# Kernel tuning notes

Hardware: AMD Instinct MI355X
Metric: run time of the kernel (lower is better)

Reference implementation:

```python
import jax, jax.numpy as jnp
import numpy as np

B, N, M, D, H = 4, 512, 4096, 256, 8
HD = D // H


def setup_inputs() -> dict:
    key = jax.random.key(0)
    ks = jax.random.split(key, 10)
    s = 1.0 / np.sqrt(D)
    return {
        "amr_feats": jax.random.normal(ks[0], (B, N, D), jnp.float32),
        "amr_pad_mask": jax.random.randint(ks[1], (B, N), 0, 2) == 1,
        "visual_feats": jax.random.normal(ks[2], (B, M, D), jnp.float32),
        "W_amr_qk": jax.random.normal(ks[3], (D, D), jnp.float32) * s,
        "W_amr_v": jax.random.normal(ks[4], (D, D), jnp.float32) * s,
        "W_vis_qk": jax.random.normal(ks[5], (D, D), jnp.float32) * s,
        "W_vis_v": jax.random.normal(ks[6], (D, D), jnp.float32) * s,
        "W_amr_out": jax.random.normal(ks[7], (D, D), jnp.float32) * s,
        "b_amr_out": jnp.zeros((D,), jnp.float32),
        "W_vis_out": jax.random.normal(ks[8], (D, D), jnp.float32) * s,
        "b_vis_out": jnp.zeros((D,), jnp.float32),
    }


def _split_heads(x):  # [b, s, d] -> [b, h, s, hd]
    b, s, _ = x.shape
    return x.reshape(b, s, H, HD).transpose(0, 2, 1, 3)


def _merge_heads(x):  # [b, h, s, hd] -> [b, s, d]
    b, _, s, _ = x.shape
    return x.transpose(0, 2, 1, 3).reshape(b, s, H * HD)


def reference(amr_feats, amr_pad_mask, visual_feats,
              W_amr_qk, W_amr_v, W_vis_qk, W_vis_v,
              W_amr_out, b_amr_out, W_vis_out, b_vis_out):
    scale = HD ** -0.5
    amr_qk = _split_heads(amr_feats @ W_amr_qk)      # [b,h,n,hd]
    vis_qk = _split_heads(visual_feats @ W_vis_qk)   # [b,h,m,hd]
    amr_v = _split_heads(amr_feats @ W_amr_v)        # [b,h,n,hd]
    vis_v = _split_heads(visual_feats @ W_vis_v)     # [b,h,m,hd]

    # shared score matrix, computed once and reused for both directions
    common = jnp.einsum('bhnc,bhmc->bhnm', amr_qk, vis_qk) * scale  # [b,h,n,m]

    # amr -> visual (visual_pads is None in the top-level forward: no mask)
    amr_vis_w = jax.nn.softmax(common, axis=-1)
    amr_feats_2 = _merge_heads(jnp.einsum('bhnm,bhmc->bhnc', amr_vis_w, vis_v))
    amr_feats_2 = amr_feats_2 @ W_amr_out + b_amr_out

    # visual -> amr, masked by amr_pad_mask
    neg = jnp.finfo(common.dtype).min
    vis_txt = jnp.where(amr_pad_mask[:, None, None, :], neg,
                        common.transpose(0, 1, 3, 2))  # [b,h,m,n]
    vis_txt_w = jax.nn.softmax(vis_txt, axis=-1)
    visual_feats_2 = _merge_heads(jnp.einsum('bhmn,bhnc->bhmc', vis_txt_w, amr_v))
    visual_feats_2 = visual_feats_2 @ W_vis_out + b_vis_out

    # text_trans == 'dot', visual_trans == 'dot'
    return amr_feats_2 * amr_feats, visual_feats * visual_feats_2
```

## Files before the change

### kernel.cpp

```cpp
#include <hip/hip_runtime.h>

#define BB 4
#define NN 512
#define MM 4096
#define DD 256
#define HH 8
#define HDD 32

typedef __attribute__((ext_vector_type(8))) short bf16x8;
typedef __attribute__((ext_vector_type(4))) float f32x4;
typedef __attribute__((ext_vector_type(4))) unsigned int u32x4;

__device__ __forceinline__ unsigned short f2b(float f) {
    union { float f; unsigned u; } v; v.f = f;
    unsigned r = v.u + 0x7fffu + ((v.u >> 16) & 1u);
    return (unsigned short)(r >> 16);
}
__device__ __forceinline__ float b2f(unsigned short u) {
    union { unsigned u; float f; } v; v.u = ((unsigned)u) << 16;
    return v.f;
}
__device__ __forceinline__ unsigned cvt_pk_bf16(float lo, float hi) {
    unsigned r;
    asm("v_cvt_pk_bf16_f32 %0, %1, %2" : "=v"(r) : "v"(lo), "v"(hi));
    return r;
}

struct WPack { const float* s[6]; unsigned short* d[6]; };
__global__ __launch_bounds__(256) void convert_w(WPack p)
{
    __shared__ unsigned short T[64][72];
    const int mat = blockIdx.x >> 4;
    const int tile = blockIdx.x & 15;
    const int kt = (tile >> 2) * 64, ct = (tile & 3) * 64;
    const int t = threadIdx.x;
    const int kl = t >> 2, cseg = (t & 3) * 16;

    const float* src = &p.s[mat][(size_t)(kt + kl) * DD + ct + cseg];
    #pragma unroll
    for (int j4 = 0; j4 < 4; ++j4) {
        const float4 f = *(const float4*)(src + j4 * 4);
        T[cseg + j4 * 4 + 0][kl] = f2b(f.x);
        T[cseg + j4 * 4 + 1][kl] = f2b(f.y);
        T[cseg + j4 * 4 + 2][kl] = f2b(f.z);
        T[cseg + j4 * 4 + 3][kl] = f2b(f.w);
    }
    __syncthreads();
    unsigned short* dst = &p.d[mat][(size_t)(ct + kl) * DD + kt + cseg];
    *(bf16x8*)dst       = *(const bf16x8*)&T[kl][cseg];
    *(bf16x8*)(dst + 8) = *(const bf16x8*)&T[kl][cseg + 8];
}

template<int OUTMODE>
__device__ __forceinline__ void gemm_tile_in(
    const float* __restrict__ A,
    const unsigned short* __restrict__ Wt,
    float outscale,
    unsigned short* __restrict__ Cb,
    unsigned short* __restrict__ VT, int SEQ,
    const int* __restrict__ rowmask,
    int r0, int c0,
    unsigned short (*As)[72], unsigned short (*Ws)[72])
{
    const int tid = threadIdx.x;
    const int lane = tid & 63, w = tid >> 6;
    const int rq = (w >> 1) * 32, cq = (w & 1) * 32;
    const int srow = tid >> 2, skc = (tid & 3) * 16;
    const int g = lane >> 4, cl = lane & 15;

    f32x4 acc[2][2] = {};

    for (int ks = 0; ks < DD; ks += 64) {
        __syncthreads();
        {
            const float* ga = &A[(size_t)(r0 + srow) * DD + ks + skc];
            const float4 f0 = *(const float4*)(ga);
            const float4 f1 = *(const float4*)(ga + 4);
            const float4 f2 = *(const float4*)(ga + 8);
            const float4 f3 = *(const float4*)(ga + 12);
            uint4 u0, u1;
            u0.x = cvt_pk_bf16(f0.x, f0.y); u0.y = cvt_pk_bf16(f0.z, f0.w);
            u0.z = cvt_pk_bf16(f1.x, f1.y); u0.w = cvt_pk_bf16(f1.z, f1.w);
            u1.x = cvt_pk_bf16(f2.x, f2.y); u1.y = cvt_pk_bf16(f2.z, f2.w);
            u1.z = cvt_pk_bf16(f3.x, f3.y); u1.w = cvt_pk_bf16(f3.z, f3.w);
            *(uint4*)&As[srow][skc]     = u0;
            *(uint4*)&As[srow][skc + 8] = u1;
            const unsigned short* gw = &Wt[(size_t)(c0 + srow) * DD + ks + skc];
            *(bf16x8*)&Ws[srow][skc]     = *(const bf16x8*)gw;
            *(bf16x8*)&Ws[srow][skc + 8] = *(const bf16x8*)(gw + 8);
        }
        __syncthreads();
        #pragma unroll
        for (int kh = 0; kh < 2; ++kh) {
            const int kk = kh * 32 + g * 8;
            const bf16x8 a0 = *(const bf16x8*)&As[rq + cl][kk];
            const bf16x8 a1 = *(const bf16x8*)&As[rq + 16 + cl][kk];
            const bf16x8 b0 = *(const bf16x8*)&Ws[cq + cl][kk];
            const bf16x8 b1 = *(const bf16x8*)&Ws[cq + 16 + cl][kk];
            acc[0][0] = __builtin_amdgcn_mfma_f32_16x16x32_bf16(a0, b0, acc[0][0], 0, 0, 0);
            acc[0][1] = __builtin_amdgcn_mfma_f32_16x16x32_bf16(a0, b1, acc[0][1], 0, 0, 0);
            acc[1][0] = __builtin_amdgcn_mfma_f32_16x16x32_bf16(a1, b0, acc[1][0], 0, 0, 0);
            acc[1][1] = __builtin_amdgcn_mfma_f32_16x16x32_bf16(a1, b1, acc[1][1], 0, 0, 0);
        }
    }

    if (OUTMODE == 0) {
        const int b0 = r0 / SEQ, mbase = r0 % SEQ;
        #pragma unroll
        for (int sr = 0; sr < 2; ++sr)
        #pragma unroll
        for (int sc = 0; sc < 2; ++sc) {
            const int col = c0 + cq + sc * 16 + cl;
            const int head = col >> 5, c32 = col & 31;
            #pragma unroll
            for (int reg = 0; reg < 4; ++reg) {
                const int m = mbase + rq + sr * 16 + g * 4 + reg;
                Cb[(((size_t)b0 * HH + head) * SEQ + m) * 32 + c32]
                    = f2b(acc[sr][sc][reg] * outscale);
            }
        }
    } else {
        const int b0 = r0 / SEQ, mbase = r0 % SEQ;
        if (rowmask != nullptr) {
            #pragma unroll
            for (int sr = 0; sr < 2; ++sr)
                #pragma unroll
                for (int reg = 0; reg < 4; ++reg) {
                    const int m = mbase + rq + sr * 16 + g * 4 + reg;
                    const float k = rowmask[b0 * SEQ + m] ? 0.f : 1.f;
                    acc[sr][0][reg] *= k;
                    acc[sr][1][reg] *= k;
                }
        }
        __syncthreads();
        #pragma unroll
        for (int sr = 0; sr < 2; ++sr)
        #pragma unroll
        for (int sc = 0; sc < 2; ++sc) {
            const int col_local = cq + sc * 16 + cl;
            uint2 u;
            u.x = cvt_pk_bf16(acc[sr][sc][0], acc[sr][sc][1]);
            u.y = cvt_pk_bf16(acc[sr][sc][2], acc[sr][sc][3]);
            *(uint2*)&As[col_local][rq + g * 8 + sr * 4] = u;
        }
        __syncthreads();
        const int col = tid >> 2, seg = tid & 3;
        unsigned short* dst = &VT[((size_t)b0 * DD + c0 + col) * SEQ + mbase + seg * 16];
        *(bf16x8*)dst       = *(const bf16x8*)&As[col][seg * 16];
        *(bf16x8*)(dst + 8) = *(const bf16x8*)&As[col][seg * 16 + 8];
    }
}

struct InPack {
    const float* amr; const float* vis;
    const unsigned short *Wqa, *Wva, *Wqv, *Wvv;
    unsigned short *amr_qk, *vis_qk, *VTa, *VTv;
    const int* mask;
    unsigned short* keepP;
    float sqs;
};
__global__ __launch_bounds__(256) void gemm_in(InPack p)
{
    __shared__ unsigned short As[64][72];
    __shared__ unsigned short Ws[64][72];
    const int bx = blockIdx.x;
    const int c0 = blockIdx.y * 64;
    if (bx < 32)
        gemm_tile_in<0>(p.amr, p.Wqa, p.sqs, p.amr_qk, nullptr, NN, nullptr, bx * 64, c0, As, Ws);
    else if (bx < 64)
        gemm_tile_in<2>(p.amr, p.Wva, 1.f, nullptr, p.VTa, NN, p.mask, (bx - 32) * 64, c0, As, Ws);
    else if (bx < 320)
        gemm_tile_in<0>(p.vis, p.Wqv, p.sqs, p.vis_qk, nullptr, MM, nullptr, (bx - 64) * 64, c0, As, Ws);
    else if (bx < 576)
        gemm_tile_in<2>(p.vis, p.Wvv, 1.f, nullptr, p.VTv, MM, nullptr, (bx - 320) * 64, c0, As, Ws);
    else if (blockIdx.y == 0) {
        #pragma unroll
        for (int k8 = 0; k8 < 8; ++k8) {
            const int idx = k8 * 256 + threadIdx.x;
            const int m = idx & (NN - 1);
            const int r = m & 31;
            const int pp = ((r & 15) >> 2) * 8 + (r >> 4) * 4 + (r & 3);
            p.keepP[(idx & ~(NN - 1)) | (m & ~31) | pp]
                = p.mask[idx] ? (unsigned short)0 : (unsigned short)0x3F80;
        }
    }
}

__device__ __forceinline__ void gemm_tile_out(
    const unsigned short* __restrict__ A,
    const unsigned short* __restrict__ Wt,
    const float* __restrict__ bias,
    const float* __restrict__ feats,
    float* __restrict__ Cf,
    int r0, int c0,
    unsigned short (*As)[72], unsigned short (*Ws)[72])
{
    const int tid = threadIdx.x;
    const int lane = tid & 63, w = tid >> 6;
    const int rq = (w >> 1) * 32, cq = (w & 1) * 32;
    const int srow = tid >> 2, skc = (tid & 3) * 16;
    const int g = lane >> 4, cl = lane & 15;

    f32x4 acc[2][2] = {};

    for (int ks = 0; ks < DD; ks += 64) {
        __syncthreads();
        {
            const unsigned short* ga = &A[(size_t)(r0 + srow) * DD + ks + skc];
            *(bf16x8*)&As[srow][skc]     = *(const bf16x8*)ga;
            *(bf16x8*)&As[srow][skc + 8] = *(const bf16x8*)(ga + 8);
            const unsigned short* gw = &Wt[(size_t)(c0 + srow) * DD + ks + skc];
            *(bf16x8*)&Ws[srow][skc]     = *(const bf16x8*)gw;
            *(bf16x8*)&Ws[srow][skc + 8] = *(const bf16x8*)(gw + 8);
        }
        __syncthreads();
        #pragma unroll
        for (int kh = 0; kh < 2; ++kh) {
            const int kk = kh * 32 + g * 8;
            const bf16x8 a0 = *(const bf16x8*)&As[rq + cl][kk];
            const bf16x8 a1 = *(const bf16x8*)&As[rq + 16 + cl][kk];
            const bf16x8 b0 = *(const bf16x8*)&Ws[cq + cl][kk];
            const bf16x8 b1 = *(const bf16x8*)&Ws[cq + 16 + cl][kk];
            acc[0][0] = __builtin_amdgcn_mfma_f32_16x16x32_bf16(a0, b0, acc[0][0], 0, 0, 0);
            acc[0][1] = __builtin_amdgcn_mfma_f32_16x16x32_bf16(a0, b1, acc[0][1], 0, 0, 0);
            acc[1][0] = __builtin_amdgcn_mfma_f32_16x16x32_bf16(a1, b0, acc[1][0], 0, 0, 0);
            acc[1][1] = __builtin_amdgcn_mfma_f32_16x16x32_bf16(a1, b1, acc[1][1], 0, 0, 0);
        }
    }

    #pragma unroll
    for (int sr = 0; sr < 2; ++sr)
    #pragma unroll
    for (int sc = 0; sc < 2; ++sc) {
        const int col = c0 + cq + sc * 16 + cl;
        #pragma unroll
        for (int reg = 0; reg < 4; ++reg) {
            const int row = r0 + rq + sr * 16 + g * 4 + reg;
            const size_t idx = (size_t)row * DD + col;
            Cf[idx] = (acc[sr][sc][reg] + bias[col]) * feats[idx];
        }
    }
}

struct OutPack {
    const unsigned short* A[2];
    const unsigned short* Wt[2];
    const float* bias[2];
    const float* feats[2];
    float* O[2];
};
__global__ __launch_bounds__(256) void gemm_out(OutPack p)
{
    __shared__ unsigned short As[64][72];
    __shared__ unsigned short Ws[64][72];
    const int bx = blockIdx.x;
    const int which = (bx < 32) ? 0 : 1;
    const int rb = (bx < 32) ? bx : bx - 32;
    gemm_tile_out(p.A[which], p.Wt[which], p.bias[which], p.feats[which],
                  p.O[which], rb * 64, blockIdx.y * 64, As, Ws);
}

template<int SEQK, int SPLIT, bool HAS_KEEP>
__device__ __forceinline__ void attn_body(
    int bid,
    const unsigned short* __restrict__ Qb,
    const unsigned short* __restrict__ Kb,
    const unsigned short* __restrict__ VTb,
    const unsigned short* __restrict__ keepP,
    unsigned short* __restrict__ ctx,
    float* __restrict__ Pl, unsigned short* __restrict__ PaccB,
    int NQ)
{
    constexpr int KCHUNK = SEQK / SPLIT;
    constexpr int NT = KCHUNK / 64;

    const int tid = threadIdx.x;
    const int lane = tid & 63, w = tid >> 6;
    const int g = lane >> 4, cl = lane & 15;

    const int nqt = NQ / 256;
    int bi = bid;
    const int sp = bi % SPLIT; bi /= SPLIT;
    const int qt = bi % nqt;   bi /= nqt;
    const int h  = bi % HH;
    const int b  = bi / HH;
    const int q0 = qt * 256 + w * 64;
    const int kv0 = sp * KCHUNK;

    bf16x8 aq[4];
    #pragma unroll
    for (int qg = 0; qg < 4; ++qg)
        aq[qg] = *(const bf16x8*)
            &Qb[(((size_t)b * HH + h) * NQ + q0 + qg * 16 + cl) * 32 + g * 8];

    const unsigned short* Kp0 = Kb + (((size_t)b * HH + h) * SEQK + kv0 + cl) * 32 + g * 8;
    const unsigned short* Vp0 = VTb + ((size_t)b * DD + h * HDD + cl) * SEQK + kv0 + g * 8;
    const unsigned short* Op0 = HAS_KEEP ? (keepP + (size_t)b * SEQK + kv0 + g * 8) : nullptr;

    union { u32x4 u; bf16x8 b; } onesc;
    onesc.u[0] = 0x3F803F80u; onesc.u[1] = 0x3F803F80u;
    onesc.u[2] = 0x3F803F80u; onesc.u[3] = 0x3F803F80u;

    f32x4 acc[4][2] = {};
    f32x4 acc_l[4] = {};

    bf16x8 Kc[4], Kn[4];
    #pragma unroll
    for (int kf = 0; kf < 4; ++kf)
        Kc[kf] = *(const bf16x8*)(Kp0 + (size_t)(kf * 16) * 32);

    for (int t = 0; t < NT; ++t) {
        if (t + 1 < NT) {
            const unsigned short* kp = Kp0 + (size_t)((t + 1) * 64) * 32;
            #pragma unroll
            for (int kf = 0; kf < 4; ++kf)
                Kn[kf] = *(const bf16x8*)(kp + (size_t)(kf * 16) * 32);
        }

        bf16x8 vv[2][2];
        #pragma unroll
        for (int mh = 0; mh < 2; ++mh)
            #pragma unroll
            for (int sub = 0; sub < 2; ++sub)
                vv[mh][sub] = *(const bf16x8*)
                    (Vp0 + (size_t)(sub * 16) * SEQK + t * 64 + mh * 32);

        bf16x8 ofrag[2];
        if (HAS_KEEP) {
            ofrag[0] = *(const bf16x8*)(Op0 + t * 64);
            ofrag[1] = *(const bf16x8*)(Op0 + t * 64 + 32);
        } else {
            ofrag[0] = onesc.b;
            ofrag[1] = onesc.b;
        }

        uint2 X[4][4];
        #pragma unroll
        for (int kh = 0; kh < 2; ++kh) {
            f32x4 s[4][2];
            #pragma unroll
            for (int k2 = 0; k2 < 2; ++k2) {
                const f32x4 z = {0.f, 0.f, 0.f, 0.f};
                const bf16x8 kfrag = Kc[kh * 2 + k2];
                #pragma unroll
                for (int qg = 0; qg < 4; ++qg)
                    s[qg][k2] = __builtin_amdgcn_mfma_f32_16x16x32_bf16(
                        kfrag, aq[qg], z, 0, 0, 0);
            }
            #pragma unroll
            for (int k2 = 0; k2 < 2; ++k2) {
                const int kf = kh * 2 + k2;
                #pragma unroll
                for (int qg = 0; qg < 4; ++qg) {
                    const float p0 = exp2f(s[qg][k2][0]);
                    const float p1 = exp2f(s[qg][k2][1]);
                    const float p2 = exp2f(s[qg][k2][2]);
                    const float p3 = exp2f(s[qg][k2][3]);
                    X[qg][kf].x = cvt_pk_bf16(p0, p1);
                    X[qg][kf].y = cvt_pk_bf16(p2, p3);
                }
            }
        }

        #pragma unroll
        for (int mh = 0; mh < 2; ++mh) {
            union { u32x4 u; bf16x8 b; } pa[4];
            #pragma unroll
            for (int qg = 0; qg < 4; ++qg) {
                pa[qg].u[0] = X[qg][mh * 2].x;
                pa[qg].u[1] = X[qg][mh * 2].y;
                pa[qg].u[2] = X[qg][mh * 2 + 1].x;
                pa[qg].u[3] = X[qg][mh * 2 + 1].y;
            }
            #pragma unroll
            for (int sub = 0; sub < 2; ++sub)
                #pragma unroll
                for (int qg = 0; qg < 4; ++qg)
                    acc[qg][sub] = __builtin_amdgcn_mfma_f32_16x16x32_bf16(
                        pa[qg].b, vv[mh][sub], acc[qg][sub], 0, 0, 0);
            #pragma unroll
            for (int qg = 0; qg < 4; ++qg)
                acc_l[qg] = __builtin_amdgcn_mfma_f32_16x16x32_bf16(
                    pa[qg].b, ofrag[mh], acc_l[qg], 0, 0, 0);
        }

        #pragma unroll
        for (int kf = 0; kf < 4; ++kf) Kc[kf] = Kn[kf];
    }

    if (SPLIT > 1) {
        const int pb = bid;
        #pragma unroll
        for (int qg = 0; qg < 4; ++qg) {
            #pragma unroll
            for (int sub = 0; sub < 2; ++sub)
                #pragma unroll
                for (int reg = 0; reg < 4; ++reg) {
                    const int wq = w * 64 + qg * 16 + g * 4 + reg;
                    PaccB[((size_t)pb * 256 + wq) * 32 + sub * 16 + cl]
                        = f2b(acc[qg][sub][reg]);
                }
            if (cl == 0) {
                #pragma unroll
                for (int reg = 0; reg < 4; ++reg)
                    Pl[(size_t)pb * 256 + w * 64 + qg * 16 + g * 4 + reg]
                        = acc_l[qg][reg];
            }
        }
    } else {
        #pragma unroll
        for (int qg = 0; qg < 4; ++qg)
            #pragma unroll
            for (int sub = 0; sub < 2; ++sub)
                #pragma unroll
                for (int reg = 0; reg < 4; ++reg) {
                    const int q = q0 + qg * 16 + g * 4 + reg;
                    ctx[((size_t)b * NQ + q) * DD + h * HDD + sub * 16 + cl]
                        = f2b(acc[qg][sub][reg] / acc_l[qg][reg]);
                }
    }
}

__global__ __launch_bounds__(256) void attn_fused(
    const unsigned short* __restrict__ amr_qk,
    const unsigned short* __restrict__ vis_qk,
    const unsigned short* __restrict__ VT_vis,
    const unsigned short* __restrict__ VT_amr,
    const unsigned short* __restrict__ keepP,
    unsigned short* __restrict__ ctx1,
    float* __restrict__ Pl, unsigned short* __restrict__ PaccB)
{
    if ((blockIdx.x & 1) == 0) {
        attn_body<MM, 8, false>(blockIdx.x >> 1, amr_qk, vis_qk, VT_vis, nullptr,
                                nullptr, Pl, PaccB, NN);
    } else {
        attn_body<NN, 1, true>(blockIdx.x >> 1, vis_qk, amr_qk, VT_amr, keepP,
                               ctx1, nullptr, nullptr, MM);
    }
}

__global__ __launch_bounds__(256) void combine_split(
    const float* __restrict__ Pl, const unsigned short* __restrict__ PaccB,
    unsigned short* __restrict__ ctx)
{
    const int q = threadIdx.x;
    const int bqt = blockIdx.x;
    const int qt = bqt & 1, h = (bqt >> 1) & 7, b = bqt >> 4;
    const int pb0 = bqt * 8;

    float denom = 0.f;
    float o[32] = {};
    #pragma unroll
    for (int sp = 0; sp < 8; ++sp) {
        const size_t base = ((size_t)(pb0 + sp) * 256 + q) * 32;
        #pragma unroll
        for (int c8 = 0; c8 < 4; ++c8) {
            const bf16x8 a = *(const bf16x8*)&PaccB[base + c8 * 8];
            #pragma unroll
            for (int j = 0; j < 8; ++j)
                o[c8 * 8 + j] += b2f((unsigned short)a[j]);
        }
        denom += Pl[(size_t)(pb0 + sp) * 256 + q];
    }
    const float inv = 1.f / denom;

    unsigned short* dst = &ctx[((size_t)b * NN + qt * 256 + q) * DD + h * HDD];
    #pragma unroll
    for (int j4 = 0; j4 < 8; ++j4) {
        ushort4 u;
        u.x = f2b(o[j4 * 4 + 0] * inv); u.y = f2b(o[j4 * 4 + 1] * inv);
        u.z = f2b(o[j4 * 4 + 2] * inv); u.w = f2b(o[j4 * 4 + 3] * inv);
        *(ushort4*)(dst + j4 * 4) = u;
    }
}

extern "C" void kernel_launch(void* const* d_in, const int* in_sizes, int n_in,
                              void* d_out, int out_size, void* d_ws, size_t ws_size,
                              hipStream_t stream)
{
    const float* amr_feats    = (const float*)d_in[0];
    const int*   amr_pad_mask = (const int*)d_in[1];
    const float* visual_feats = (const float*)d_in[2];
    const float* W_amr_qk     = (const float*)d_in[3];
    const float* W_amr_v      = (const float*)d_in[4];
    const float* W_vis_qk     = (const float*)d_in[5];
    const float* W_vis_v      = (const float*)d_in[6];
    const float* W_amr_out    = (const float*)d_in[7];
    const float* b_amr_out    = (const float*)d_in[8];
    const float* W_vis_out    = (const float*)d_in[9];
    const float* b_vis_out    = (const float*)d_in[10];

    unsigned short* ws = (unsigned short*)d_ws;
    unsigned short* Wt_amr_qk  = ws;
    unsigned short* Wt_amr_v   = ws + 65536;
    unsigned short* Wt_vis_qk  = ws + 131072;
    unsigned short* Wt_vis_v   = ws + 196608;
    unsigned short* Wt_amr_out = ws + 262144;
    unsigned short* Wt_vis_out = ws + 327680;
    unsigned short* amr_qk_b   = ws + 393216;
    unsigned short* VT_amr     = ws + 917504;
    unsigned short* vis_qk_b   = ws + 1441792;
    unsigned short* VT_vis     = ws + 5636096;
    unsigned short* ctx0_b     = ws + 9830400;
    unsigned short* ctx1_b     = ws + 10354688;
    float* Pl                  = (float*)(ws + 14548992);
    unsigned short* PaccB      = ws + 15073280;
    unsigned short* keepP      = ws + 19267584;

    float* out0 = (float*)d_out;
    float* out1 = out0 + (size_t)BB * NN * DD;

    const float SQS = 0.50500976f;

    WPack wp;
    wp.s[0] = W_amr_qk;  wp.d[0] = Wt_amr_qk;
    wp.s[1] = W_amr_v;   wp.d[1] = Wt_amr_v;
    wp.s[2] = W_vis_qk;  wp.d[2] = Wt_vis_qk;
    wp.s[3] = W_vis_v;   wp.d[3] = Wt_vis_v;
    wp.s[4] = W_amr_out; wp.d[4] = Wt_amr_out;
    wp.s[5] = W_vis_out; wp.d[5] = Wt_vis_out;
    convert_w<<<96, 256, 0, stream>>>(wp);

    InPack ip;
    ip.amr = amr_feats; ip.vis = visual_feats;
    ip.Wqa = Wt_amr_qk; ip.Wva = Wt_amr_v;
    ip.Wqv = Wt_vis_qk; ip.Wvv = Wt_vis_v;
    ip.amr_qk = amr_qk_b; ip.vis_qk = vis_qk_b;
    ip.VTa = VT_amr; ip.VTv = VT_vis;
    ip.mask = amr_pad_mask; ip.keepP = keepP;
    ip.sqs = SQS;
    gemm_in<<<dim3(577, 4), 256, 0, stream>>>(ip);

    attn_fused<<<1024, 256, 0, stream>>>(
        amr_qk_b, vis_qk_b, VT_vis, VT_amr, keepP, ctx1_b, Pl, PaccB);
    combine_split<<<64, 256, 0, stream>>>(Pl, PaccB, ctx0_b);

    OutPack op;
    op.A[0] = ctx0_b; op.Wt[0] = Wt_amr_out; op.bias[0] = b_amr_out;
    op.feats[0] = amr_feats;    op.O[0] = out0;
    op.A[1] = ctx1_b; op.Wt[1] = Wt_vis_out; op.bias[1] = b_vis_out;
    op.feats[1] = visual_feats; op.O[1] = out1;
    gemm_out<<<dim3(288, 4), 256, 0, stream>>>(op);
}
```

Baseline: 91.85 us.

## Fuse QK/V input projections per tile and shrink attention blocks to one wave

The input projection kernel now computes the QK and V projections in the same block, loading and converting each activation tile once and running two weight tiles against it. The attention kernel goes from 256-thread blocks covering 256 queries to 64-thread single-wave blocks covering 64 queries, with four times as many blocks, and the exp/convert is interleaved per k-half instead of buffered. The combine kernel is reshaped to match, with each thread handling an 8-column slice. This cuts redundant activation reads and raises block-level parallelism and scheduling flexibility, at the cost of more register pressure in the fused GEMM and more, smaller blocks. The visual-side attention path (attn_body with NQ=MM) may also be affected by the nqt change, which could be inconsistent with code not shown.

```diff
diff --git a/kernel.cpp b/kernel.cpp
--- a/kernel.cpp
+++ b/kernel.cpp
@@ -51,24 +51,55 @@
     *(bf16x8*)(dst + 8) = *(const bf16x8*)&T[kl][cseg + 8];
 }
 
-template<int OUTMODE>
-__device__ __forceinline__ void gemm_tile_in(
-    const float* __restrict__ A,
-    const unsigned short* __restrict__ Wt,
-    float outscale,
-    unsigned short* __restrict__ Cb,
-    unsigned short* __restrict__ VT, int SEQ,
-    const int* __restrict__ rowmask,
-    int r0, int c0,
-    unsigned short (*As)[72], unsigned short (*Ws)[72])
-{
+struct InPack {
+    const float* amr; const float* vis;
+    const unsigned short *Wqa, *Wva, *Wqv, *Wvv;
+    unsigned short *amr_qk, *vis_qk, *VTa, *VTv;
+    const int* mask;
+    unsigned short* keepP;
+    float sqs;
+};
+__global__ __launch_bounds__(256) void gemm_in(InPack p)
+{
+    __shared__ unsigned short As[64][72];
+    __shared__ unsigned short Wq[64][72];
+    __shared__ unsigned short Wv[64][72];
+
+    const int bx = blockIdx.x;
+    if (bx == 288) {
+        if (blockIdx.y == 0) {
+            #pragma unroll
+            for (int k8 = 0; k8 < 8; ++k8) {
+                const int idx = k8 * 256 + threadIdx.x;
+                const int m = idx & (NN - 1);
+                const int r = m & 31;
+                const int pp = ((r & 15) >> 2) * 8 + (r >> 4) * 4 + (r & 3);
+                p.keepP[(idx & ~(NN - 1)) | (m & ~31) | pp]
+                    = p.mask[idx] ? (unsigned short)0 : (unsigned short)0x3F80;
+            }
+        }
+        return;
+    }
+
+    const float* A; const unsigned short *Wqm, *Wvm;
+    unsigned short *Cq, *VT; const int* rowmask; int SEQ, r0;
+    if (bx < 32) {
+        A = p.amr; Wqm = p.Wqa; Wvm = p.Wva; Cq = p.amr_qk; VT = p.VTa;
+        rowmask = p.mask; SEQ = NN; r0 = bx * 64;
+    } else {
+        A = p.vis; Wqm = p.Wqv; Wvm = p.Wvv; Cq = p.vis_qk; VT = p.VTv;
+        rowmask = nullptr; SEQ = MM; r0 = (bx - 32) * 64;
+    }
+    const int c0 = blockIdx.y * 64;
+
     const int tid = threadIdx.x;
     const int lane = tid & 63, w = tid >> 6;
     const int rq = (w >> 1) * 32, cq = (w & 1) * 32;
     const int srow = tid >> 2, skc = (tid & 3) * 16;
     const int g = lane >> 4, cl = lane & 15;
 
-    f32x4 acc[2][2] = {};
+    f32x4 aq[2][2] = {};
+    f32x4 av[2][2] = {};
 
     for (int ks = 0; ks < DD; ks += 64) {
         __syncthreads();
@@ -85,6 +116,104 @@
             u1.z = cvt_pk_bf16(f3.x, f3.y); u1.w = cvt_pk_bf16(f3.z, f3.w);
             *(uint4*)&As[srow][skc]     = u0;
             *(uint4*)&As[srow][skc + 8] = u1;
+            const unsigned short* gq = &Wqm[(size_t)(c0 + srow) * DD + ks + skc];
+            *(bf16x8*)&Wq[srow][skc]     = *(const bf16x8*)gq;
+            *(bf16x8*)&Wq[srow][skc + 8] = *(const bf16x8*)(gq + 8);
+            const unsigned short* gv = &Wvm[(size_t)(c0 + srow) * DD + ks + skc];
+            *(bf16x8*)&Wv[srow][skc]     = *(const bf16x8*)gv;
+            *(bf16x8*)&Wv[srow][skc + 8] = *(const bf16x8*)(gv + 8);
+        }
+        __syncthreads();
+        #pragma unroll
+        for (int kh = 0; kh < 2; ++kh) {
+            const int kk = kh * 32 + g * 8;
+            const bf16x8 a0 = *(const bf16x8*)&As[rq + cl][kk];
+            const bf16x8 a1 = *(const bf16x8*)&As[rq + 16 + cl][kk];
+            const bf16x8 q0 = *(const bf16x8*)&Wq[cq + cl][kk];
+            const bf16x8 q1 = *(const bf16x8*)&Wq[cq + 16 + cl][kk];
+            const bf16x8 v0 = *(const bf16x8*)&Wv[cq + cl][kk];
+            const bf16x8 v1 = *(const bf16x8*)&Wv[cq + 16 + cl][kk];
+            aq[0][0] = __builtin_amdgcn_mfma_f32_16x16x32_bf16(a0, q0, aq[0][0], 0, 0, 0);
+            aq[0][1] = __builtin_amdgcn_mfma_f32_16x16x32_bf16(a0, q1, aq[0][1], 0, 0, 0);
+            aq[1][0] = __builtin_amdgcn_mfma_f32_16x16x32_bf16(a1, q0, aq[1][0], 0, 0, 0);
+            aq[1][1] = __builtin_amdgcn_mfma_f32_16x16x32_bf16(a1, q1, aq[1][1], 0, 0, 0);
+            av[0][0] = __builtin_amdgcn_mfma_f32_16x16x32_bf16(a0, v0, av[0][0], 0, 0, 0);
+            av[0][1] = __builtin_amdgcn_mfma_f32_16x16x32_bf16(a0, v1, av[0][1], 0, 0, 0);
+            av[1][0] = __builtin_amdgcn_mfma_f32_16x16x32_bf16(a1, v0, av[1][0], 0, 0, 0);
+            av[1][1] = __builtin_amdgcn_mfma_f32_16x16x32_bf16(a1, v1, av[1][1], 0, 0, 0);
+        }
+    }
+
+    const int b0 = r0 / SEQ, mbase = r0 % SEQ;
+
+    #pragma unroll
+    for (int sr = 0; sr < 2; ++sr)
+    #pragma unroll
+    for (int sc = 0; sc < 2; ++sc) {
+        const int col = c0 + cq + sc * 16 + cl;
+        const int head = col >> 5, c32 = col & 31;
+        #pragma unroll
+        for (int reg = 0; reg < 4; ++reg) {
+            const int m = mbase + rq + sr * 16 + g * 4 + reg;
+            Cq[(((size_t)b0 * HH + head) * SEQ + m) * 32 + c32]
+                = f2b(aq[sr][sc][reg] * p.sqs);
+        }
+    }
+
+    if (rowmask != nullptr) {
+        #pragma unroll
+        for (int sr = 0; sr < 2; ++sr)
+            #pragma unroll
+            for (int reg = 0; reg < 4; ++reg) {
+                const int m = mbase + rq + sr * 16 + g * 4 + reg;
+                const float k = rowmask[b0 * SEQ + m] ? 0.f : 1.f;
+                av[sr][0][reg] *= k;
+                av[sr][1][reg] *= k;
+            }
+    }
+    __syncthreads();
+    #pragma unroll
+    for (int sr = 0; sr < 2; ++sr)
+    #pragma unroll
+    for (int sc = 0; sc < 2; ++sc) {
+        const int col_local = cq + sc * 16 + cl;
+        uint2 u;
+        u.x = cvt_pk_bf16(av[sr][sc][0], av[sr][sc][1]);
+        u.y = cvt_pk_bf16(av[sr][sc][2], av[sr][sc][3]);
+        *(uint2*)&As[col_local][rq + g * 8 + sr * 4] = u;
+    }
+    __syncthreads();
+    {
+        const int col = tid >> 2, seg = tid & 3;
+        unsigned short* dst = &VT[((size_t)b0 * DD + c0 + col) * SEQ + mbase + seg * 16];
+        *(bf16x8*)dst       = *(const bf16x8*)&As[col][seg * 16];
+        *(bf16x8*)(dst + 8) = *(const bf16x8*)&As[col][seg * 16 + 8];
+    }
+}
+
+__device__ __forceinline__ void gemm_tile_out(
+    const unsigned short* __restrict__ A,
+    const unsigned short* __restrict__ Wt,
+    const float* __restrict__ bias,
+    const float* __restrict__ feats,
+    float* __restrict__ Cf,
+    int r0, int c0,
+    unsigned short (*As)[72], unsigned short (*Ws)[72])
+{
+    const int tid = threadIdx.x;
+    const int lane = tid & 63, w = tid >> 6;
+    const int rq = (w >> 1) * 32, cq = (w & 1) * 32;
+    const int srow = tid >> 2, skc = (tid & 3) * 16;
+    const int g = lane >> 4, cl = lane & 15;
+
+    f32x4 acc[2][2] = {};
+
+    for (int ks = 0; ks < DD; ks += 64) {
+        __syncthreads();
+        {
+            const unsigned short* ga = &A[(size_t)(r0 + srow) * DD + ks + skc];
+            *(bf16x8*)&As[srow][skc]     = *(const bf16x8*)ga;
+            *(bf16x8*)&As[srow][skc + 8] = *(const bf16x8*)(ga + 8);
             const unsigned short* gw = &Wt[(size_t)(c0 + srow) * DD + ks + skc];
             *(bf16x8*)&Ws[srow][skc]     = *(const bf16x8*)gw;
             *(bf16x8*)&Ws[srow][skc + 8] = *(const bf16x8*)(gw + 8);
@@ -104,130 +233,6 @@
         }
     }
 
-    if (OUTMODE == 0) {
-        const int b0 = r0 / SEQ, mbase = r0 % SEQ;
-        #pragma unroll
-        for (int sr = 0; sr < 2; ++sr)
-        #pragma unroll
-        for (int sc = 0; sc < 2; ++sc) {
-            const int col = c0 + cq + sc * 16 + cl;
-            const int head = col >> 5, c32 = col & 31;
-            #pragma unroll
-            for (int reg = 0; reg < 4; ++reg) {
-                const int m = mbase + rq + sr * 16 + g * 4 + reg;
-                Cb[(((size_t)b0 * HH + head) * SEQ + m) * 32 + c32]
-                    = f2b(acc[sr][sc][reg] * outscale);
-            }
-        }
-    } else {
-        const int b0 = r0 / SEQ, mbase = r0 % SEQ;
-        if (rowmask != nullptr) {
-            #pragma unroll
-            for (int sr = 0; sr < 2; ++sr)
-                #pragma unroll
-                for (int reg = 0; reg < 4; ++reg) {
-                    const int m = mbase + rq + sr * 16 + g * 4 + reg;
-                    const float k = rowmask[b0 * SEQ + m] ? 0.f : 1.f;
-                    acc[sr][0][reg] *= k;
-                    acc[sr][1][reg] *= k;
-                }
-        }
-        __syncthreads();
-        #pragma unroll
-        for (int sr = 0; sr < 2; ++sr)
-        #pragma unroll
-        for (int sc = 0; sc < 2; ++sc) {
-            const int col_local = cq + sc * 16 + cl;
-            uint2 u;
-            u.x = cvt_pk_bf16(acc[sr][sc][0], acc[sr][sc][1]);
-            u.y = cvt_pk_bf16(acc[sr][sc][2], acc[sr][sc][3]);
-            *(uint2*)&As[col_local][rq + g * 8 + sr * 4] = u;
-        }
-        __syncthreads();
-        const int col = tid >> 2, seg = tid & 3;
-        unsigned short* dst = &VT[((size_t)b0 * DD + c0 + col) * SEQ + mbase + seg * 16];
-        *(bf16x8*)dst       = *(const bf16x8*)&As[col][seg * 16];
-        *(bf16x8*)(dst + 8) = *(const bf16x8*)&As[col][seg * 16 + 8];
-    }
-}
-
-struct InPack {
-    const float* amr; const float* vis;
-    const unsigned short *Wqa, *Wva, *Wqv, *Wvv;
-    unsigned short *amr_qk, *vis_qk, *VTa, *VTv;
-    const int* mask;
-    unsigned short* keepP;
-    float sqs;
-};
-__global__ __launch_bounds__(256) void gemm_in(InPack p)
-{
-    __shared__ unsigned short As[64][72];
-    __shared__ unsigned short Ws[64][72];
-    const int bx = blockIdx.x;
-    const int c0 = blockIdx.y * 64;
-    if (bx < 32)
-        gemm_tile_in<0>(p.amr, p.Wqa, p.sqs, p.amr_qk, nullptr, NN, nullptr, bx * 64, c0, As, Ws);
-    else if (bx < 64)
-        gemm_tile_in<2>(p.amr, p.Wva, 1.f, nullptr, p.VTa, NN, p.mask, (bx - 32) * 64, c0, As, Ws);
-    else if (bx < 320)
-        gemm_tile_in<0>(p.vis, p.Wqv, p.sqs, p.vis_qk, nullptr, MM, nullptr, (bx - 64) * 64, c0, As, Ws);
-    else if (bx < 576)
-        gemm_tile_in<2>(p.vis, p.Wvv, 1.f, nullptr, p.VTv, MM, nullptr, (bx - 320) * 64, c0, As, Ws);
-    else if (blockIdx.y == 0) {
-        #pragma unroll
-        for (int k8 = 0; k8 < 8; ++k8) {
-            const int idx = k8 * 256 + threadIdx.x;
-            const int m = idx & (NN - 1);
-            const int r = m & 31;
-            const int pp = ((r & 15) >> 2) * 8 + (r >> 4) * 4 + (r & 3);
-            p.keepP[(idx & ~(NN - 1)) | (m & ~31) | pp]
-                = p.mask[idx] ? (unsigned short)0 : (unsigned short)0x3F80;
-        }
-    }
-}
-
-__device__ __forceinline__ void gemm_tile_out(
-    const unsigned short* __restrict__ A,
-    const unsigned short* __restrict__ Wt,
-    const float* __restrict__ bias,
-    const float* __restrict__ feats,
-    float* __restrict__ Cf,
-    int r0, int c0,
-    unsigned short (*As)[72], unsigned short (*Ws)[72])
-{
-    const int tid = threadIdx.x;
-    const int lane = tid & 63, w = tid >> 6;
-    const int rq = (w >> 1) * 32, cq = (w & 1) * 32;
-    const int srow = tid >> 2, skc = (tid & 3) * 16;
-    const int g = lane >> 4, cl = lane & 15;
-
-    f32x4 acc[2][2] = {};
-
-    for (int ks = 0; ks < DD; ks += 64) {
-        __syncthreads();
-        {
-            const unsigned short* ga = &A[(size_t)(r0 + srow) * DD + ks + skc];
-            *(bf16x8*)&As[srow][skc]     = *(const bf16x8*)ga;
-            *(bf16x8*)&As[srow][skc + 8] = *(const bf16x8*)(ga + 8);
-            const unsigned short* gw = &Wt[(size_t)(c0 + srow) * DD + ks + skc];
-            *(bf16x8*)&Ws[srow][skc]     = *(const bf16x8*)gw;
-            *(bf16x8*)&Ws[srow][skc + 8] = *(const bf16x8*)(gw + 8);
-        }
-        __syncthreads();
-        #pragma unroll
-        for (int kh = 0; kh < 2; ++kh) {
-            const int kk = kh * 32 + g * 8;
-            const bf16x8 a0 = *(const bf16x8*)&As[rq + cl][kk];
-            const bf16x8 a1 = *(const bf16x8*)&As[rq + 16 + cl][kk];
-            const bf16x8 b0 = *(const bf16x8*)&Ws[cq + cl][kk];
-            const bf16x8 b1 = *(const bf16x8*)&Ws[cq + 16 + cl][kk];
-            acc[0][0] = __builtin_amdgcn_mfma_f32_16x16x32_bf16(a0, b0, acc[0][0], 0, 0, 0);
-            acc[0][1] = __builtin_amdgcn_mfma_f32_16x16x32_bf16(a0, b1, acc[0][1], 0, 0, 0);
-            acc[1][0] = __builtin_amdgcn_mfma_f32_16x16x32_bf16(a1, b0, acc[1][0], 0, 0, 0);
-            acc[1][1] = __builtin_amdgcn_mfma_f32_16x16x32_bf16(a1, b1, acc[1][1], 0, 0, 0);
-        }
-    }
-
     #pragma unroll
     for (int sr = 0; sr < 2; ++sr)
     #pragma unroll
@@ -274,17 +279,16 @@
     constexpr int KCHUNK = SEQK / SPLIT;
     constexpr int NT = KCHUNK / 64;
 
-    const int tid = threadIdx.x;
-    const int lane = tid & 63, w = tid >> 6;
+    const int lane = threadIdx.x & 63;
     const int g = lane >> 4, cl = lane & 15;
 
-    const int nqt = NQ / 256;
+    const int nqt = NQ / 64;
     int bi = bid;
     const int sp = bi % SPLIT; bi /= SPLIT;
     const int qt = bi % nqt;   bi /= nqt;
     const int h  = bi % HH;
     const int b  = bi / HH;
-    const int q0 = qt * 256 + w * 64;
+    const int q0 = qt * 64;
     const int kv0 = sp * KCHUNK;
 
     bf16x8 aq[4];
@@ -334,7 +338,6 @@
             ofrag[1] = onesc.b;
         }
 
-        uint2 X[4][4];
         #pragma unroll
         for (int kh = 0; kh < 2; ++kh) {
             f32x4 s[4][2];
@@ -347,41 +350,24 @@
                     s[qg][k2] = __builtin_amdgcn_mfma_f32_16x16x32_bf16(
                         kfrag, aq[qg], z, 0, 0, 0);
             }
-            #pragma unroll
-            for (int k2 = 0; k2 < 2; ++k2) {
-                const int kf = kh * 2 + k2;
-                #pragma unroll
-                for (int qg = 0; qg < 4; ++qg) {
-                    const float p0 = exp2f(s[qg][k2][0]);
-                    const float p1 = exp2f(s[qg][k2][1]);
-                    const float p2 = exp2f(s[qg][k2][2]);
-                    const float p3 = exp2f(s[qg][k2][3]);
-                    X[qg][kf].x = cvt_pk_bf16(p0, p1);
-                    X[qg][kf].y = cvt_pk_bf16(p2, p3);
-                }
-            }
-        }
-
-        #pragma unroll
-        for (int mh = 0; mh < 2; ++mh) {
             union { u32x4 u; bf16x8 b; } pa[4];
             #pragma unroll
             for (int qg = 0; qg < 4; ++qg) {
-                pa[qg].u[0] = X[qg][mh * 2].x;
-                pa[qg].u[1] = X[qg][mh * 2].y;
-                pa[qg].u[2] = X[qg][mh * 2 + 1].x;
-                pa[qg].u[3] = X[qg][mh * 2 + 1].y;
+                pa[qg].u[0] = cvt_pk_bf16(exp2f(s[qg][0][0]), exp2f(s[qg][0][1]));
+                pa[qg].u[1] = cvt_pk_bf16(exp2f(s[qg][0][2]), exp2f(s[qg][0][3]));
+                pa[qg].u[2] = cvt_pk_bf16(exp2f(s[qg][1][0]), exp2f(s[qg][1][1]));
+                pa[qg].u[3] = cvt_pk_bf16(exp2f(s[qg][1][2]), exp2f(s[qg][1][3]));
             }
             #pragma unroll
             for (int sub = 0; sub < 2; ++sub)
                 #pragma unroll
                 for (int qg = 0; qg < 4; ++qg)
                     acc[qg][sub] = __builtin_amdgcn_mfma_f32_16x16x32_bf16(
-                        pa[qg].b, vv[mh][sub], acc[qg][sub], 0, 0, 0);
+                        pa[qg].b, vv[kh][sub], acc[qg][sub], 0, 0, 0);
             #pragma unroll
             for (int qg = 0; qg < 4; ++qg)
                 acc_l[qg] = __builtin_amdgcn_mfma_f32_16x16x32_bf16(
-                    pa[qg].b, ofrag[mh], acc_l[qg], 0, 0, 0);
+                    pa[qg].b, ofrag[kh], acc_l[qg], 0, 0, 0);
         }
 
         #pragma unroll
@@ -396,15 +382,14 @@
             for (int sub = 0; sub < 2; ++sub)
                 #pragma unroll
                 for (int reg = 0; reg < 4; ++reg) {
-                    const int wq = w * 64 + qg * 16 + g * 4 + reg;
-                    PaccB[((size_t)pb * 256 + wq) * 32 + sub * 16 + cl]
+                    const int wq = qg * 16 + g * 4 + reg;
+                    PaccB[((size_t)pb * 64 + wq) * 32 + sub * 16 + cl]
                         = f2b(acc[qg][sub][reg]);
                 }
             if (cl == 0) {
                 #pragma unroll
                 for (int reg = 0; reg < 4; ++reg)
-                    Pl[(size_t)pb * 256 + w * 64 + qg * 16 + g * 4 + reg]
-                        = acc_l[qg][reg];
+                    Pl[(size_t)pb * 64 + qg * 16 + g * 4 + reg] = acc_l[qg][reg];
             }
         }
     } else {
@@ -421,7 +406,7 @@
     }
 }
 
-__global__ __launch_bounds__(256) void attn_fused(
+__global__ __launch_bounds__(64) void attn_fused(
     const unsigned short* __restrict__ amr_qk,
     const unsigned short* __restrict__ vis_qk,
     const unsigned short* __restrict__ VT_vis,
@@ -443,35 +428,33 @@
     const float* __restrict__ Pl, const unsigned short* __restrict__ PaccB,
     unsigned short* __restrict__ ctx)
 {
-    const int q = threadIdx.x;
+    const int t = threadIdx.x;
+    const int q = t >> 2, cseg = (t & 3) * 8;
     const int bqt = blockIdx.x;
-    const int qt = bqt & 1, h = (bqt >> 1) & 7, b = bqt >> 4;
+    const int qt = bqt & 7, h = (bqt >> 3) & 7, b = bqt >> 6;
     const int pb0 = bqt * 8;
 
     float denom = 0.f;
-    float o[32] = {};
+    float o[8] = {};
     #pragma unroll
     for (int sp = 0; sp < 8; ++sp) {
-        const size_t base = ((size_t)(pb0 + sp) * 256 + q) * 32;
-        #pragma unroll
-        for (int c8 = 0; c8 < 4; ++c8) {
-            const bf16x8 a = *(const bf16x8*)&PaccB[base + c8 * 8];
-            #pragma unroll
-            for (int j = 0; j < 8; ++j)
-                o[c8 * 8 + j] += b2f((unsigned short)a[j]);
-        }
-        denom += Pl[(size_t)(pb0 + sp) * 256 + q];
+        const size_t base = ((size_t)(pb0 + sp) * 64 + q) * 32 + cseg;
+        const bf16x8 a = *(const bf16x8*)&PaccB[base];
+        #pragma unroll
+        for (int j = 0; j < 8; ++j)
+            o[j] += b2f((unsigned short)a[j]);
+        denom += Pl[(size_t)(pb0 + sp) * 64 + q];
     }
     const float inv = 1.f / denom;
 
-    unsigned short* dst = &ctx[((size_t)b * NN + qt * 256 + q) * DD + h * HDD];
-    #pragma unroll
-    for (int j4 = 0; j4 < 8; ++j4) {
-        ushort4 u;
-        u.x = f2b(o[j4 * 4 + 0] * inv); u.y = f2b(o[j4 * 4 + 1] * inv);
-        u.z = f2b(o[j4 * 4 + 2] * inv); u.w = f2b(o[j4 * 4 + 3] * inv);
-        *(ushort4*)(dst + j4 * 4) = u;
-    }
+    unsigned short* dst = &ctx[((size_t)b * NN + qt * 64 + q) * DD + h * HDD + cseg];
+    ushort4 u0, u1;
+    u0.x = f2b(o[0] * inv); u0.y = f2b(o[1] * inv);
+    u0.z = f2b(o[2] * inv); u0.w = f2b(o[3] * inv);
+    u1.x = f2b(o[4] * inv); u1.y = f2b(o[5] * inv);
+    u1.z = f2b(o[6] * inv); u1.w = f2b(o[7] * inv);
+    *(ushort4*)dst       = u0;
+    *(ushort4*)(dst + 4) = u1;
 }
 
 extern "C" void kernel_launch(void* const* d_in, const int* in_sizes, int n_in,
@@ -529,11 +512,11 @@
     ip.VTa = VT_amr; ip.VTv = VT_vis;
     ip.mask = amr_pad_mask; ip.keepP = keepP;
     ip.sqs = SQS;
-    gemm_in<<<dim3(577, 4), 256, 0, stream>>>(ip);
-
-    attn_fused<<<1024, 256, 0, stream>>>(
+    gemm_in<<<dim3(289, 4), 256, 0, stream>>>(ip);
+
+    attn_fused<<<4096, 64, 0, stream>>>(
         amr_qk_b, vis_qk_b, VT_vis, VT_amr, keepP, ctx1_b, Pl, PaccB);
-    combine_split<<<64, 256, 0, stream>>>(Pl, PaccB, ctx0_b);
+    combine_split<<<256, 256, 0, stream>>>(Pl, PaccB, ctx0_b);
 
     OutPack op;
     op.A[0] = ctx0_b; op.Wt[0] = Wt_amr_out; op.bias[0] = b_amr_out;
```

New measurement: 88.37 us. 3.8% less time.
